# Performance work log

Hardware: AMD Instinct MI355X
Metric: run time of the kernel (lower is better)

## Reference

```python
import jax, jax.numpy as jnp
import numpy as np

DIM = 768
HEADS = 12
DIM_HEAD = DIM // HEADS  # 64
INNER = DIM_HEAD * HEADS  # 768
HIDDEN = 4 * DIM  # 3072
N = 31  # num_patches + 1, fixed by Block (num_patches=30)
B = 512
EPS = 1e-5
MASK_VAL = -987654321.0


def layernorm(x, g, b):
    mu = jnp.mean(x, axis=-1, keepdims=True)
    var = jnp.mean(jnp.square(x - mu), axis=-1, keepdims=True)
    return (x - mu) * jax.lax.rsqrt(var + EPS) * g + b


def setup_inputs() -> dict:
    key = jax.random.key(0)
    ks = jax.random.split(key, 12)
    s = 0.02
    return {
        "x": jax.random.normal(ks[0], (B, N, DIM), jnp.float32),
        "ln1_g": jnp.ones((DIM,), jnp.float32),
        "ln1_b": jnp.zeros((DIM,), jnp.float32),
        "w_qkv": jax.random.normal(ks[1], (DIM, 3 * INNER), jnp.float32) * s,
        "scale": jnp.full((HEADS,), DIM_HEAD ** -0.5, jnp.float32),
        "w_o": jax.random.normal(ks[2], (INNER, DIM), jnp.float32) * s,
        "b_o": jnp.zeros((DIM,), jnp.float32),
        "ln2_g": jnp.ones((DIM,), jnp.float32),
        "ln2_b": jnp.zeros((DIM,), jnp.float32),
        "w1": jax.random.normal(ks[3], (DIM, HIDDEN), jnp.float32) * s,
        "b1": jnp.zeros((HIDDEN,), jnp.float32),
        "w2": jax.random.normal(ks[4], (HIDDEN, DIM), jnp.float32) * s,
        "b2": jnp.zeros((DIM,), jnp.float32),
    }


def reference(x, ln1_g, ln1_b, w_qkv, scale, w_o, b_o, ln2_g, ln2_b, w1, b1, w2, b2):
    b, n, _ = x.shape
    # --- LSA attention ---
    h = layernorm(x, ln1_g, ln1_b)
    qkv = h @ w_qkv  # [b, n, 3*inner]
    q, k, v = jnp.split(qkv, 3, axis=-1)
    def split_heads(t):
        return t.reshape(b, n, HEADS, DIM_HEAD).transpose(0, 2, 1, 3)  # b h n d
    q, k, v = split_heads(q), split_heads(k), split_heads(v)
    dots = jnp.einsum('bhid,bhjd->bhij', q, k) * scale[None, :, None, None]
    # diagonal exclusion mask (self-token masked out)
    diag = jnp.eye(n, dtype=bool)
    dots = jnp.where(diag[None, None], MASK_VAL, dots)
    attn = jax.nn.softmax(dots, axis=-1)
    out = jnp.einsum('bhij,bhjd->bhid', attn, v)
    out = out.transpose(0, 2, 1, 3).reshape(b, n, INNER)
    x = x + out @ w_o + b_o
    # --- MLP ---
    h2 = layernorm(x, ln2_g, ln2_b)
    h2 = jax.nn.gelu(h2 @ w1 + b1, approximate=False)
    x = x + h2 @ w2 + b2
    return x
```

## Files before the change

kernel.cpp:

```cpp
#include <hip/hip_runtime.h>
#include <math.h>

#define DIM 768
#define HEADS 12
#define DHEAD 64
#define NTOK 31
#define BATCH 512
#define MTOK (BATCH * NTOK)
#define HIDDEN 3072
#define QKVN 2304
#define MASK_VAL -987654321.0f

typedef short s16x8 __attribute__((ext_vector_type(8)));
typedef float f32x4 __attribute__((ext_vector_type(4)));

static __device__ __forceinline__ float bs2f(unsigned short u) {
  unsigned int x = ((unsigned int)u) << 16;
  return __builtin_bit_cast(float, x);
}
static __device__ __forceinline__ unsigned short f2bs(float f) {
  unsigned int x = __builtin_bit_cast(unsigned int, f);
  x += 0x7fffu + ((x >> 16) & 1u);
  return (unsigned short)(x >> 16);
}

static __device__ __forceinline__ void gload16(const unsigned short* g, unsigned short* l) {
  __builtin_amdgcn_global_load_lds(
      (const __attribute__((address_space(1))) unsigned int*)g,
      (__attribute__((address_space(3))) unsigned int*)l, 16, 0, 0);
}

static __device__ __forceinline__ float epi_apply(int EPI, float v, int col, size_t idx,
                                                  const float* bias, const void* resid) {
  if (EPI == 0) return v;
  if (EPI == 2) {
    float t = v + bias[col];
    float arg = 1.5957691216f * t * (1.f + 0.044715f * t * t);
    return t * __builtin_amdgcn_rcpf(1.f + __expf(-arg));
  }
  if (EPI == 3) return v + bias[col] + ((const float*)resid)[idx];
  return v + bias[col] + bs2f(((const unsigned short*)resid)[idx]);
}

static __device__ __forceinline__ void epi_store(int EPI, void* outp, size_t idx, float t) {
  if (EPI == 4) ((float*)outp)[idx] = t;
  else ((unsigned short*)outp)[idx] = f2bs(t);
}

__global__ __launch_bounds__(256) void transpose_all_kernel(
    const float* __restrict__ w_qkv, const float* __restrict__ w_o,
    const float* __restrict__ w1, const float* __restrict__ w2,
    unsigned short* __restrict__ wqkvT, unsigned short* __restrict__ woT,
    unsigned short* __restrict__ w1T, unsigned short* __restrict__ w2T) {
  int t = blockIdx.x;
  const float* w;
  unsigned short* wt;
  int K, N, tx;
  if (t < 432) { w = w_qkv; wt = wqkvT; K = DIM; N = QKVN; tx = QKVN / 64; }
  else if (t < 576) { t -= 432; w = w_o; wt = woT; K = DIM; N = DIM; tx = DIM / 64; }
  else if (t < 1152) { t -= 576; w = w1; wt = w1T; K = DIM; N = HIDDEN; tx = HIDDEN / 64; }
  else { t -= 1152; w = w2; wt = w2T; K = HIDDEN; N = DIM; tx = DIM / 64; }
  int n0 = (t % tx) * 64, k0 = (t / tx) * 64;

  __shared__ float tl[64][65];
  int tid = threadIdx.x;
  int r = tid >> 4, c4 = (tid & 15) * 4;
#pragma unroll
  for (int i = 0; i < 4; ++i) {
    float4 v = *(const float4*)(w + (size_t)(k0 + r + i * 16) * N + n0 + c4);
    tl[r + i * 16][c4] = v.x;
    tl[r + i * 16][c4 + 1] = v.y;
    tl[r + i * 16][c4 + 2] = v.z;
    tl[r + i * 16][c4 + 3] = v.w;
  }
  __syncthreads();
#pragma unroll
  for (int i = 0; i < 4; ++i) {
    int n = r + i * 16;
    ushort4 o;
    o.x = f2bs(tl[c4 + 0][n]);
    o.y = f2bs(tl[c4 + 1][n]);
    o.z = f2bs(tl[c4 + 2][n]);
    o.w = f2bs(tl[c4 + 3][n]);
    *(ushort4*)(wt + (size_t)(n0 + n) * K + k0 + c4) = o;
  }
}

__global__ __launch_bounds__(256) void ln_kernel(const float* __restrict__ x,
                                                 const float* __restrict__ g,
                                                 const float* __restrict__ bta,
                                                 unsigned short* __restrict__ out) {
  int wid = threadIdx.x >> 6, lane = threadIdx.x & 63;
  size_t row = (size_t)blockIdx.x * 4 + wid;
  const float4* xr = (const float4*)(x + row * DIM);
  float4 v[3];
  v[0] = xr[lane];
  v[1] = xr[lane + 64];
  v[2] = xr[lane + 128];
  float s = 0.f, sq = 0.f;
#pragma unroll
  for (int i = 0; i < 3; ++i) {
    s += v[i].x + v[i].y + v[i].z + v[i].w;
    sq += v[i].x * v[i].x + v[i].y * v[i].y + v[i].z * v[i].z + v[i].w * v[i].w;
  }
#pragma unroll
  for (int off = 32; off; off >>= 1) {
    s += __shfl_xor(s, off);
    sq += __shfl_xor(sq, off);
  }
  float mu = s * (1.f / DIM);
  float var = sq * (1.f / DIM) - mu * mu;
  float rs = rsqrtf(var + 1e-5f);
#pragma unroll
  for (int i = 0; i < 3; ++i) {
    int col = i * 256 + lane * 4;
    float4 gg = *(const float4*)(g + col);
    float4 bb = *(const float4*)(bta + col);
    ushort4 o;
    o.x = f2bs((v[i].x - mu) * rs * gg.x + bb.x);
    o.y = f2bs((v[i].y - mu) * rs * gg.y + bb.y);
    o.z = f2bs((v[i].z - mu) * rs * gg.z + bb.z);
    o.w = f2bs((v[i].w - mu) * rs * gg.w + bb.w);
    *(ushort4*)(out + row * DIM + col) = o;
  }
}

__global__ __launch_bounds__(256) void ln_bf16_kernel(const unsigned short* __restrict__ x,
                                                      const float* __restrict__ g,
                                                      const float* __restrict__ bta,
                                                      unsigned short* __restrict__ out) {
  int wid = threadIdx.x >> 6, lane = threadIdx.x & 63;
  size_t row = (size_t)blockIdx.x * 4 + wid;
  const unsigned short* xr = x + row * DIM;
  float v[12];
#pragma unroll
  for (int i = 0; i < 3; ++i) {
    ushort4 u = *(const ushort4*)(xr + i * 256 + lane * 4);
    v[i * 4 + 0] = bs2f(u.x);
    v[i * 4 + 1] = bs2f(u.y);
    v[i * 4 + 2] = bs2f(u.z);
    v[i * 4 + 3] = bs2f(u.w);
  }
  float s = 0.f, sq = 0.f;
#pragma unroll
  for (int i = 0; i < 12; ++i) {
    s += v[i];
    sq += v[i] * v[i];
  }
#pragma unroll
  for (int off = 32; off; off >>= 1) {
    s += __shfl_xor(s, off);
    sq += __shfl_xor(sq, off);
  }
  float mu = s * (1.f / DIM);
  float var = sq * (1.f / DIM) - mu * mu;
  float rs = rsqrtf(var + 1e-5f);
#pragma unroll
  for (int i = 0; i < 3; ++i) {
    int col = i * 256 + lane * 4;
    float4 gg = *(const float4*)(g + col);
    float4 bb = *(const float4*)(bta + col);
    ushort4 o;
    o.x = f2bs((v[i * 4 + 0] - mu) * rs * gg.x + bb.x);
    o.y = f2bs((v[i * 4 + 1] - mu) * rs * gg.y + bb.y);
    o.z = f2bs((v[i * 4 + 2] - mu) * rs * gg.z + bb.z);
    o.w = f2bs((v[i * 4 + 3] - mu) * rs * gg.w + bb.w);
    *(ushort4*)(out + row * DIM + col) = o;
  }
}

template <int CMH, int CS, int CB, int RBUF, int RMH, int RKH, int RB, int VM, int NORD,
          typename STF>
__device__ __forceinline__ void gphP(const char* aB0, const char* bKH0, const char* bKH1,
                                     s16x8 (&af2)[2][4], s16x8 (&bk2)[2][3],
                                     f32x4 (&acc)[8][3], STF&& stage) {
  stage();
  if (VM == 2) asm volatile("s_waitcnt vmcnt(2)");
  if (VM == 0) asm volatile("s_waitcnt vmcnt(0)");
  __builtin_amdgcn_s_barrier();
  if (!NORD) {
    const char* aP = aB0 + RBUF * 32768 + RKH * 16384 + RMH * 4096;
#pragma unroll
    for (int mi = 0; mi < 4; ++mi) af2[CS ^ 1][mi] = *(const s16x8*)(aP + mi * 1024);
    if (RMH == 0) {
      const char* bp = (RKH ? bKH1 : bKH0) + RBUF * 24576;
#pragma unroll
      for (int ni = 0; ni < 3; ++ni) bk2[RB][ni] = *(const s16x8*)(bp + ni * 2048);
    }
  }
  __builtin_amdgcn_s_setprio(1);
#pragma unroll
  for (int mi = 0; mi < 4; ++mi)
#pragma unroll
    for (int ni = 0; ni < 3; ++ni)
      acc[CMH * 4 + mi][ni] = __builtin_amdgcn_mfma_f32_16x16x32_bf16(
          af2[CS][mi], bk2[CB][ni], acc[CMH * 4 + mi][ni], 0, 0, 0);
  __builtin_amdgcn_s_setprio(0);
  __builtin_amdgcn_s_barrier();
}

template <int EPI, int TPB>
__device__ __forceinline__ void gemm192_body(
    const unsigned short* __restrict__ A, const unsigned short* __restrict__ Bt,
    void* __restrict__ outp, const float* __restrict__ bias,
    const void* __restrict__ resid, int M, int N, int K, int ntn) {
  __shared__ char ldsc[114688];
  int tid = threadIdx.x;
  int lane = tid & 63, w = tid >> 6;
  int wm = w >> 2, wn = w & 3;
  int fr = lane & 15, q = lane >> 4;

  int nwg = gridDim.x, orig = blockIdx.x;
  int qd = nwg >> 3, r8 = nwg & 7, xcd = orig & 7, loc = orig >> 3;
  int bid = (xcd < r8 ? xcd * (qd + 1) : r8 * (qd + 1) + (xcd - r8) * qd) + loc;

  int rdoffA = (q * 16) ^ (((fr >> 1) & 3) << 4);
  const char* aB0 = ldsc + (wm * 128 + fr) * 64 + rdoffA;
  int brow0 = wn * 48 + fr;
  int bsw = brow0 & 7;
  const char* bBase = ldsc + 65536 + brow0 * 128 + (q ^ (bsw & 3)) * 16;
  const char* bKH0 = bBase + ((0 ^ (bsw >> 2)) * 64);
  const char* bKH1 = bBase + ((1 ^ (bsw >> 2)) * 64);

  int srow = tid >> 2;
  int seoffA = (((tid & 3) ^ ((srow >> 1) & 3))) << 3;
  size_t rstep = (size_t)K * 256;
  int NT = K / 64;

#pragma unroll 1
  for (int tl = 0; tl < TPB; ++tl) {
    int tile = bid * TPB + tl;
    int m0 = (tile / ntn) * 256, n0 = (tile % ntn) * 192;

    const char* Ab = (const char*)A + ((size_t)(m0 + srow) * K + seoffA) * 2;
    const char* Bb2 = (const char*)Bt +
        ((size_t)(n0 + (tid >> 3)) * K + (((tid & 7) ^ ((tid >> 3) & 7)) * 8)) * 2;

    auto stgA = [&](int kh, int buf, int t) {
      const char* gp = Ab + t * 128 + kh * 64;
      unsigned short* lp = (unsigned short*)(ldsc + buf * 32768 + kh * 16384 + w * 1024);
      gload16((const unsigned short*)gp, lp);
      gload16((const unsigned short*)(gp + rstep), (unsigned short*)((char*)lp + 8192));
    };
    auto stgB = [&](int j, int buf, int t) {
      gload16((const unsigned short*)(Bb2 + (size_t)j * 128 * K + t * 128),
              (unsigned short*)(ldsc + 65536 + buf * 24576 + j * 8192 + w * 1024));
    };
    auto nop = [&] {};

    f32x4 acc[8][3] = {};
    s16x8 af2[2][4], bk2[2][3];

    stgA(0, 0, 0);
    stgA(1, 0, 0);
    stgB(0, 0, 0);
    stgB(1, 0, 0);
    stgB(2, 0, 0);
    stgA(0, 1, 1);
    asm volatile("s_waitcnt vmcnt(2)");
    __builtin_amdgcn_s_barrier();
    {
#pragma unroll
      for (int mi = 0; mi < 4; ++mi) af2[0][mi] = *(const s16x8*)(aB0 + mi * 1024);
#pragma unroll
      for (int ni = 0; ni < 3; ++ni) bk2[0][ni] = *(const s16x8*)(bKH0 + ni * 2048);
    }

    for (int t = 0; t + 3 < NT; t += 2) {
      gphP<0, 0, 0, 0, 1, 0, 0, -1, 0>(aB0, bKH0, bKH1, af2, bk2, acc,
          [&] { stgA(1, 1, t + 1); stgB(0, 1, t + 1); stgB(1, 1, t + 1); });
      gphP<1, 1, 0, 0, 0, 1, 1, -1, 0>(aB0, bKH0, bKH1, af2, bk2, acc,
          [&] { stgB(2, 1, t + 1); });
      gphP<0, 0, 1, 0, 1, 1, 0, -1, 0>(aB0, bKH0, bKH1, af2, bk2, acc,
          [&] { stgA(0, 0, t + 2); });
      gphP<1, 1, 1, 1, 0, 0, 0, 2, 0>(aB0, bKH0, bKH1, af2, bk2, acc, nop);
      gphP<0, 0, 0, 1, 1, 0, 0, -1, 0>(aB0, bKH0, bKH1, af2, bk2, acc,
          [&] { stgA(1, 0, t + 2); stgB(0, 0, t + 2); stgB(1, 0, t + 2); });
      gphP<1, 1, 0, 1, 0, 1, 1, -1, 0>(aB0, bKH0, bKH1, af2, bk2, acc,
          [&] { stgB(2, 0, t + 2); });
      gphP<0, 0, 1, 1, 1, 1, 0, -1, 0>(aB0, bKH0, bKH1, af2, bk2, acc,
          [&] { stgA(0, 1, t + 3); });
      gphP<1, 1, 1, 0, 0, 0, 0, 2, 0>(aB0, bKH0, bKH1, af2, bk2, acc, nop);
    }
    gphP<0, 0, 0, 0, 1, 0, 0, -1, 0>(aB0, bKH0, bKH1, af2, bk2, acc,
        [&] { stgA(1, 1, NT - 1); stgB(0, 1, NT - 1); stgB(1, 1, NT - 1); });
    gphP<1, 1, 0, 0, 0, 1, 1, -1, 0>(aB0, bKH0, bKH1, af2, bk2, acc,
        [&] { stgB(2, 1, NT - 1); });
    gphP<0, 0, 1, 0, 1, 1, 0, -1, 0>(aB0, bKH0, bKH1, af2, bk2, acc, nop);
    gphP<1, 1, 1, 1, 0, 0, 0, 0, 0>(aB0, bKH0, bKH1, af2, bk2, acc, nop);
    gphP<0, 0, 0, 1, 1, 0, 0, -1, 0>(aB0, bKH0, bKH1, af2, bk2, acc, nop);
    gphP<1, 1, 0, 1, 0, 1, 1, -1, 0>(aB0, bKH0, bKH1, af2, bk2, acc, nop);
    gphP<0, 0, 1, 1, 1, 1, 0, -1, 0>(aB0, bKH0, bKH1, af2, bk2, acc, nop);
    gphP<1, 1, 1, 0, 0, 0, 0, -1, 1>(aB0, bKH0, bKH1, af2, bk2, acc, nop);

#pragma unroll
    for (int am = 0; am < 8; ++am)
#pragma unroll
      for (int ni = 0; ni < 3; ++ni)
#pragma unroll
        for (int rr = 0; rr < 4; ++rr) {
          int row = m0 + wm * 128 + am * 16 + q * 4 + rr;
          int col = n0 + wn * 48 + ni * 16 + fr;
          size_t idx = (size_t)row * N + col;
          epi_store(EPI, outp, idx, epi_apply(EPI, acc[am][ni][rr], col, idx, bias, resid));
        }
  }
}

__global__ __launch_bounds__(512, 2) void gemm_qkv(const unsigned short* A,
                                                   const unsigned short* Bt, void* o,
                                                   const float* b, const void* r, int M,
                                                   int N, int K, int ntn) {
  gemm192_body<0, 3>(A, Bt, o, b, r, M, N, K, ntn);
}
__global__ __launch_bounds__(512, 2) void gemm_mlp1(const unsigned short* A,
                                                    const unsigned short* Bt, void* o,
                                                    const float* b, const void* r, int M,
                                                    int N, int K, int ntn) {
  gemm192_body<2, 4>(A, Bt, o, b, r, M, N, K, ntn);
}
__global__ __launch_bounds__(512, 2) void gemm_proj(const unsigned short* A,
                                                    const unsigned short* Bt, void* o,
                                                    const float* b, const void* r, int M,
                                                    int N, int K, int ntn) {
  gemm192_body<3, 1>(A, Bt, o, b, r, M, N, K, ntn);
}
__global__ __launch_bounds__(512, 2) void gemm_mlp2(const unsigned short* A,
                                                    const unsigned short* Bt, void* o,
                                                    const float* b, const void* r, int M,
                                                    int N, int K, int ntn) {
  gemm192_body<4, 1>(A, Bt, o, b, r, M, N, K, ntn);
}

__global__ __launch_bounds__(256) void attn_mfma_kernel(const unsigned short* __restrict__ qkv,
                                                        const float* __restrict__ scale,
                                                        unsigned short* __restrict__ ao) {
  __shared__ unsigned short Vt[4][64][40];
  __shared__ unsigned short Pl[4][32][32];
  int wid = threadIdx.x >> 6, lane = threadIdx.x & 63;
  int pair = blockIdx.x * 4 + wid;
  int b = pair / HEADS, h = pair % HEADS;
  const unsigned short* base = qkv + (size_t)b * NTOK * QKVN + h * DHEAD;
  const unsigned short* Qp = base;
  const unsigned short* Kp = base + 768;
  const unsigned short* Vp = base + 1536;

  int c = lane & 15, q = lane >> 4;
  int oct = q * 8;

  unsigned short vcol[NTOK];
#pragma unroll
  for (int j = 0; j < NTOK; ++j) vcol[j] = Vp[(size_t)j * QKVN + lane];
#pragma unroll
  for (int j = 0; j < NTOK; ++j) Vt[wid][lane][j] = vcol[j];
  Vt[wid][lane][31] = 0;

  s16x8 kf[2][2] = {{{0}}}, qf[2][2] = {{{0}}};
#pragma unroll
  for (int t = 0; t < 2; ++t) {
    int row = t * 16 + c;
    if (row < NTOK) {
#pragma unroll
      for (int s = 0; s < 2; ++s) {
        kf[t][s] = *(const s16x8*)(Kp + (size_t)row * QKVN + s * 32 + oct);
        qf[t][s] = *(const s16x8*)(Qp + (size_t)row * QKVN + s * 32 + oct);
      }
    }
  }

  f32x4 st[2][2] = {};
#pragma unroll
  for (int jt = 0; jt < 2; ++jt)
#pragma unroll
    for (int it = 0; it < 2; ++it)
#pragma unroll
      for (int s = 0; s < 2; ++s)
        st[jt][it] =
            __builtin_amdgcn_mfma_f32_16x16x32_bf16(kf[jt][s], qf[it][s], st[jt][it], 0, 0, 0);

  float scl = scale[h];
  float p[2][2][4];
#pragma unroll
  for (int it = 0; it < 2; ++it)
#pragma unroll
    for (int jt = 0; jt < 2; ++jt)
#pragma unroll
      for (int r = 0; r < 4; ++r) {
        int j = jt * 16 + 4 * q + r;
        int i = it * 16 + c;
        float v = st[jt][it][r] * scl;
        if (j == 31 || j == i) v = MASK_VAL;
        p[it][jt][r] = v;
      }
#pragma unroll
  for (int it = 0; it < 2; ++it) {
    float m = p[it][0][0];
#pragma unroll
    for (int jt = 0; jt < 2; ++jt)
#pragma unroll
      for (int r = 0; r < 4; ++r) m = fmaxf(m, p[it][jt][r]);
    m = fmaxf(m, __shfl_xor(m, 16));
    m = fmaxf(m, __shfl_xor(m, 32));
    float s = 0.f;
#pragma unroll
    for (int jt = 0; jt < 2; ++jt)
#pragma unroll
      for (int r = 0; r < 4; ++r) {
        float e = __expf(p[it][jt][r] - m);
        p[it][jt][r] = e;
        s += e;
      }
    s += __shfl_xor(s, 16);
    s += __shfl_xor(s, 32);
    float inv = __builtin_amdgcn_rcpf(s);
#pragma unroll
    for (int jt = 0; jt < 2; ++jt)
#pragma unroll
      for (int r = 0; r < 4; ++r) p[it][jt][r] *= inv;
  }
#pragma unroll
  for (int it = 0; it < 2; ++it)
#pragma unroll
    for (int jt = 0; jt < 2; ++jt) {
      unsigned int w0 =
          (unsigned int)f2bs(p[it][jt][0]) | ((unsigned int)f2bs(p[it][jt][1]) << 16);
      unsigned int w1 =
          (unsigned int)f2bs(p[it][jt][2]) | ((unsigned int)f2bs(p[it][jt][3]) << 16);
      uint2 pk = {w0, w1};
      *(uint2*)&Pl[wid][it * 16 + c][jt * 16 + 4 * q] = pk;
    }

  s16x8 pa[2];
#pragma unroll
  for (int it = 0; it < 2; ++it) pa[it] = *(const s16x8*)&Pl[wid][it * 16 + c][oct];
  f32x4 o[2][4];
#pragma unroll
  for (int it = 0; it < 2; ++it)
#pragma unroll
    for (int dt = 0; dt < 4; ++dt) {
      s16x8 vb = *(const s16x8*)&Vt[wid][dt * 16 + c][oct];
      f32x4 z = {0.f, 0.f, 0.f, 0.f};
      o[it][dt] = __builtin_amdgcn_mfma_f32_16x16x32_bf16(pa[it], vb, z, 0, 0, 0);
    }
#pragma unroll
  for (int it = 0; it < 2; ++it)
#pragma unroll
    for (int r = 0; r < 4; ++r) {
      int i = it * 16 + 4 * q + r;
      if (i < NTOK) {
        size_t rowoff = ((size_t)b * NTOK + i) * DIM + h * DHEAD;
#pragma unroll
        for (int dt = 0; dt < 4; ++dt) ao[rowoff + dt * 16 + c] = f2bs(o[it][dt][r]);
      }
    }
}

extern "C" void kernel_launch(void* const* d_in, const int* in_sizes, int n_in,
                              void* d_out, int out_size, void* d_ws, size_t ws_size,
                              hipStream_t stream) {
  (void)in_sizes; (void)n_in; (void)out_size; (void)ws_size;
  const float* x = (const float*)d_in[0];
  const float* ln1_g = (const float*)d_in[1];
  const float* ln1_b = (const float*)d_in[2];
  const float* w_qkv = (const float*)d_in[3];
  const float* scale = (const float*)d_in[4];
  const float* w_o = (const float*)d_in[5];
  const float* b_o = (const float*)d_in[6];
  const float* ln2_g = (const float*)d_in[7];
  const float* ln2_b = (const float*)d_in[8];
  const float* w1 = (const float*)d_in[9];
  const float* b1 = (const float*)d_in[10];
  const float* w2 = (const float*)d_in[11];
  const float* b2 = (const float*)d_in[12];

  char* ws = (char*)d_ws;
  unsigned short* buf1 = (unsigned short*)(ws + 0);
  unsigned short* qkv_bf = (unsigned short*)(ws + 24379392);
  unsigned short* x2 = (unsigned short*)(ws + 24379392);
  unsigned short* g_bf = (unsigned short*)(ws + 97517568);
  unsigned short* wqkvT = (unsigned short*)(ws + 195035136);
  unsigned short* woT = (unsigned short*)(ws + 198574080);
  unsigned short* w1T = (unsigned short*)(ws + 199753728);
  unsigned short* w2T = (unsigned short*)(ws + 204472320);

  transpose_all_kernel<<<1728, 256, 0, stream>>>(w_qkv, w_o, w1, w2, wqkvT, woT, w1T, w2T);

  ln_kernel<<<MTOK / 4, 256, 0, stream>>>(x, ln1_g, ln1_b, buf1);
  gemm_qkv<<<248, 512, 0, stream>>>(
      buf1, wqkvT, qkv_bf, nullptr, nullptr, MTOK, QKVN, DIM, QKVN / 192);
  attn_mfma_kernel<<<(BATCH * HEADS) / 4, 256, 0, stream>>>(qkv_bf, scale, buf1);
  gemm_proj<<<248, 512, 0, stream>>>(
      buf1, woT, x2, b_o, x, MTOK, DIM, DIM, DIM / 192);
  ln_bf16_kernel<<<MTOK / 4, 256, 0, stream>>>(x2, ln2_g, ln2_b, buf1);
  gemm_mlp1<<<248, 512, 0, stream>>>(
      buf1, w1T, g_bf, b1, nullptr, MTOK, HIDDEN, DIM, HIDDEN / 192);
  gemm_mlp2<<<248, 512, 0, stream>>>(
      g_bf, w2T, (float*)d_out, b2, x2, MTOK, DIM, HIDDEN, DIM / 192);
}
```

Baseline: 310.4 us.

## Add 256x256-tile GEMM body and use it for the MLP up-projection

Adds a new GEMM body that computes 256x256 output tiles with a double-buffered, 128KB LDS staging pipeline. Global loads for upcoming k-steps are interleaved with MFMA phases, using explicit vmcnt waits and barriers. The MLP first-layer GEMM switches to it, with 3 tiles per block instead of 4 tiles of 256x192. The aim is more operand reuse per loaded byte and fewer tile iterations. The cost is a larger accumulator and LDS footprint, which raises register-spill and occupancy risk under the 512-thread, 2-block launch bound.

```diff
diff --git a/kernel.cpp b/kernel.cpp
--- a/kernel.cpp
+++ b/kernel.cpp
@@ -307,6 +307,139 @@
   }
 }
 
+template <int CMH, int CS, int CB, int RBUF, int RMH, int RKH, int RB, int VM, int NORD,
+          typename STF>
+__device__ __forceinline__ void gphQ(const char* aB0, const char* bB0,
+                                     s16x8 (&af2)[2][4], s16x8 (&bk2)[2][4],
+                                     f32x4 (&acc)[8][4], STF&& stage) {
+  stage();
+  if (VM == 10) asm volatile("s_waitcnt vmcnt(10)");
+  if (VM == 4) asm volatile("s_waitcnt vmcnt(4)");
+  if (VM == 0) asm volatile("s_waitcnt vmcnt(0)");
+  __builtin_amdgcn_s_barrier();
+  if (!NORD) {
+    const char* aP = aB0 + RBUF * 32768 + RKH * 16384 + RMH * 4096;
+#pragma unroll
+    for (int mi = 0; mi < 4; ++mi) af2[CS ^ 1][mi] = *(const s16x8*)(aP + mi * 1024);
+    if (RMH == 0) {
+      const char* bP = bB0 + RBUF * 32768 + RKH * 16384;
+#pragma unroll
+      for (int ni = 0; ni < 4; ++ni) bk2[RB][ni] = *(const s16x8*)(bP + ni * 1024);
+    }
+  }
+  __builtin_amdgcn_s_setprio(1);
+#pragma unroll
+  for (int mi = 0; mi < 4; ++mi)
+#pragma unroll
+    for (int ni = 0; ni < 4; ++ni)
+      acc[CMH * 4 + mi][ni] = __builtin_amdgcn_mfma_f32_16x16x32_bf16(
+          af2[CS][mi], bk2[CB][ni], acc[CMH * 4 + mi][ni], 0, 0, 0);
+  __builtin_amdgcn_s_setprio(0);
+  __builtin_amdgcn_s_barrier();
+}
+
+template <int EPI, int TPB>
+__device__ __forceinline__ void gemm256_body(
+    const unsigned short* __restrict__ A, const unsigned short* __restrict__ Bt,
+    void* __restrict__ outp, const float* __restrict__ bias,
+    const void* __restrict__ resid, int M, int N, int K, int ntn) {
+  __shared__ char ldsc[131072];
+  int tid = threadIdx.x;
+  int lane = tid & 63, w = tid >> 6;
+  int wm = w >> 2, wn = w & 3;
+  int fr = lane & 15, q = lane >> 4;
+
+  int nwg = gridDim.x, orig = blockIdx.x;
+  int qd = nwg >> 3, r8 = nwg & 7, xcd = orig & 7, loc = orig >> 3;
+  int bid = (xcd < r8 ? xcd * (qd + 1) : r8 * (qd + 1) + (xcd - r8) * qd) + loc;
+
+  int rdoff = (q * 16) ^ (((fr >> 1) & 3) << 4);
+  const char* aB0 = ldsc + (wm * 128 + fr) * 64 + rdoff;
+  const char* bB0 = ldsc + 65536 + (wn * 64 + fr) * 64 + rdoff;
+
+  int srow = tid >> 2;
+  int seoff = (((tid & 3) ^ ((srow >> 1) & 3))) << 3;
+  size_t rstep = (size_t)K * 256;
+  int NT = K / 64;
+
+#pragma unroll 1
+  for (int tl = 0; tl < TPB; ++tl) {
+    int tile = bid * TPB + tl;
+    int m0 = (tile / ntn) * 256, n0 = (tile % ntn) * 256;
+
+    const char* Ab = (const char*)A + ((size_t)(m0 + srow) * K + seoff) * 2;
+    const char* Bb = (const char*)Bt + ((size_t)(n0 + srow) * K + seoff) * 2;
+
+    auto stg = [&](int mat, int kh, int buf, int t) {
+      const char* gp = (mat ? Bb : Ab) + t * 128 + kh * 64;
+      unsigned short* lp =
+          (unsigned short*)(ldsc + mat * 65536 + buf * 32768 + kh * 16384 + w * 1024);
+      gload16((const unsigned short*)gp, lp);
+      gload16((const unsigned short*)(gp + rstep), (unsigned short*)((char*)lp + 8192));
+    };
+    auto nop = [&] {};
+
+    f32x4 acc[8][4] = {};
+    s16x8 af2[2][4], bk2[2][4];
+
+    stg(1, 0, 0, 0);
+    stg(0, 0, 0, 0);
+    stg(1, 1, 0, 0);
+    stg(0, 1, 0, 0);
+    stg(1, 0, 1, 1);
+    stg(0, 0, 1, 1);
+    stg(1, 1, 1, 1);
+    asm volatile("s_waitcnt vmcnt(6)");
+    __builtin_amdgcn_s_barrier();
+    {
+#pragma unroll
+      for (int mi = 0; mi < 4; ++mi) af2[0][mi] = *(const s16x8*)(aB0 + mi * 1024);
+#pragma unroll
+      for (int ni = 0; ni < 4; ++ni) bk2[0][ni] = *(const s16x8*)(bB0 + ni * 1024);
+    }
+
+    for (int t = 0; t + 3 < NT; t += 2) {
+      gphQ<0, 0, 0, 0, 1, 0, 0, -1, 0>(aB0, bB0, af2, bk2, acc,
+          [&] { stg(0, 1, 1, t + 1); });
+      gphQ<1, 1, 0, 0, 0, 1, 1, 10, 0>(aB0, bB0, af2, bk2, acc,
+          [&] { stg(1, 0, 0, t + 2); });
+      gphQ<0, 0, 1, 0, 1, 1, 0, -1, 0>(aB0, bB0, af2, bk2, acc,
+          [&] { stg(0, 0, 0, t + 2); });
+      gphQ<1, 1, 1, 1, 0, 0, 0, 10, 0>(aB0, bB0, af2, bk2, acc,
+          [&] { stg(1, 1, 0, t + 2); });
+      gphQ<0, 0, 0, 1, 1, 0, 0, -1, 0>(aB0, bB0, af2, bk2, acc,
+          [&] { stg(0, 1, 0, t + 2); });
+      gphQ<1, 1, 0, 1, 0, 1, 1, 10, 0>(aB0, bB0, af2, bk2, acc,
+          [&] { stg(1, 0, 1, t + 3); });
+      gphQ<0, 0, 1, 1, 1, 1, 0, -1, 0>(aB0, bB0, af2, bk2, acc,
+          [&] { stg(0, 0, 1, t + 3); });
+      gphQ<1, 1, 1, 0, 0, 0, 0, 10, 0>(aB0, bB0, af2, bk2, acc,
+          [&] { stg(1, 1, 1, t + 3); });
+    }
+    gphQ<0, 0, 0, 0, 1, 0, 0, -1, 0>(aB0, bB0, af2, bk2, acc,
+        [&] { stg(0, 1, 1, NT - 1); });
+    gphQ<1, 1, 0, 0, 0, 1, 1, -1, 0>(aB0, bB0, af2, bk2, acc, nop);
+    gphQ<0, 0, 1, 0, 1, 1, 0, -1, 0>(aB0, bB0, af2, bk2, acc, nop);
+    gphQ<1, 1, 1, 1, 0, 0, 0, 4, 0>(aB0, bB0, af2, bk2, acc, nop);
+    gphQ<0, 0, 0, 1, 1, 0, 0, -1, 0>(aB0, bB0, af2, bk2, acc, nop);
+    gphQ<1, 1, 0, 1, 0, 1, 1, 0, 0>(aB0, bB0, af2, bk2, acc, nop);
+    gphQ<0, 0, 1, 1, 1, 1, 0, -1, 0>(aB0, bB0, af2, bk2, acc, nop);
+    gphQ<1, 1, 1, 0, 0, 0, 0, -1, 1>(aB0, bB0, af2, bk2, acc, nop);
+
+#pragma unroll
+    for (int am = 0; am < 8; ++am)
+#pragma unroll
+      for (int ni = 0; ni < 4; ++ni)
+#pragma unroll
+        for (int rr = 0; rr < 4; ++rr) {
+          int row = m0 + wm * 128 + am * 16 + q * 4 + rr;
+          int col = n0 + wn * 64 + ni * 16 + fr;
+          size_t idx = (size_t)row * N + col;
+          epi_store(EPI, outp, idx, epi_apply(EPI, acc[am][ni][rr], col, idx, bias, resid));
+        }
+  }
+}
+
 __global__ __launch_bounds__(512, 2) void gemm_qkv(const unsigned short* A,
                                                    const unsigned short* Bt, void* o,
                                                    const float* b, const void* r, int M,
@@ -317,7 +450,7 @@
                                                     const unsigned short* Bt, void* o,
                                                     const float* b, const void* r, int M,
                                                     int N, int K, int ntn) {
-  gemm192_body<2, 4>(A, Bt, o, b, r, M, N, K, ntn);
+  gemm256_body<2, 3>(A, Bt, o, b, r, M, N, K, ntn);
 }
 __global__ __launch_bounds__(512, 2) void gemm_proj(const unsigned short* A,
                                                     const unsigned short* Bt, void* o,
@@ -493,7 +626,7 @@
       buf1, woT, x2, b_o, x, MTOK, DIM, DIM, DIM / 192);
   ln_bf16_kernel<<<MTOK / 4, 256, 0, stream>>>(x2, ln2_g, ln2_b, buf1);
   gemm_mlp1<<<248, 512, 0, stream>>>(
-      buf1, w1T, g_bf, b1, nullptr, MTOK, HIDDEN, DIM, HIDDEN / 192);
+      buf1, w1T, g_bf, b1, nullptr, MTOK, HIDDEN, DIM, HIDDEN / 256);
   gemm_mlp2<<<248, 512, 0, stream>>>(
       g_bf, w2T, (float*)d_out, b2, x2, MTOK, DIM, HIDDEN, DIM / 192);
 }
```

New measurement: 308.3 us (median of 2 runs). Within noise of the previous version (-0.7%).

## Use 256x256 tile GEMM with 32x32x16 MFMA for first MLP layer

Applied to the files above, without the earlier changes.

Adds a new GEMM body that computes 256x256 output tiles per workgroup, using 32x32x16 bf16 MFMA instructions and a double-buffered 128KB LDS pipeline staged through global_load_lds. The MLP1 GEMM switches to it, covering 3 tiles per block across 248 blocks. Larger tiles raise arithmetic intensity and the bigger MFMA shape cuts LDS reads per flop. In exchange, 128KB of LDS per block limits occupancy, and tile coverage depends on M being divisible by 256.

```diff
diff --git a/kernel.cpp b/kernel.cpp
--- a/kernel.cpp
+++ b/kernel.cpp
@@ -13,6 +13,7 @@
 
 typedef short s16x8 __attribute__((ext_vector_type(8)));
 typedef float f32x4 __attribute__((ext_vector_type(4)));
+typedef float f32x16 __attribute__((ext_vector_type(16)));
 
 static __device__ __forceinline__ float bs2f(unsigned short u) {
   unsigned int x = ((unsigned int)u) << 16;
@@ -307,6 +308,126 @@
   }
 }
 
+template <int BUF, int KH, int VM, typename STF>
+__device__ __forceinline__ void gph32(const char* aB, const char* bB, int o0, int o1,
+                                      f32x16 (&acc)[4][2], STF&& stage) {
+  const char* aP = aB + BUF * 32768 + KH * 16384;
+  const char* bP = bB + BUF * 32768 + KH * 16384;
+  s16x8 af[4][2], bk[2][2];
+#pragma unroll
+  for (int mt = 0; mt < 4; ++mt) {
+    af[mt][0] = *(const s16x8*)(aP + mt * 2048 + o0);
+    af[mt][1] = *(const s16x8*)(aP + mt * 2048 + o1);
+  }
+#pragma unroll
+  for (int nt = 0; nt < 2; ++nt) {
+    bk[nt][0] = *(const s16x8*)(bP + nt * 2048 + o0);
+    bk[nt][1] = *(const s16x8*)(bP + nt * 2048 + o1);
+  }
+  stage();
+  if (VM == 8) asm volatile("s_waitcnt vmcnt(8)");
+  if (VM == 4) asm volatile("s_waitcnt vmcnt(4)");
+  if (VM == 0) asm volatile("s_waitcnt vmcnt(0)");
+  __builtin_amdgcn_s_barrier();
+  asm volatile("s_waitcnt lgkmcnt(0)");
+  __builtin_amdgcn_s_setprio(1);
+#pragma unroll
+  for (int mt = 0; mt < 4; ++mt)
+#pragma unroll
+    for (int nt = 0; nt < 2; ++nt) {
+      acc[mt][nt] =
+          __builtin_amdgcn_mfma_f32_32x32x16_bf16(af[mt][0], bk[nt][0], acc[mt][nt], 0, 0, 0);
+      acc[mt][nt] =
+          __builtin_amdgcn_mfma_f32_32x32x16_bf16(af[mt][1], bk[nt][1], acc[mt][nt], 0, 0, 0);
+    }
+  __builtin_amdgcn_s_setprio(0);
+  __builtin_amdgcn_s_barrier();
+}
+
+template <int EPI, int TPB>
+__device__ __forceinline__ void gemm256x_body(
+    const unsigned short* __restrict__ A, const unsigned short* __restrict__ Bt,
+    void* __restrict__ outp, const float* __restrict__ bias,
+    const void* __restrict__ resid, int M, int N, int K, int ntn) {
+  __shared__ char ldsc[131072];
+  int tid = threadIdx.x;
+  int lane = tid & 63, w = tid >> 6;
+  int wm = w >> 2, wn = w & 3;
+  int l31 = lane & 31, lh = lane >> 5;
+
+  int nwg = gridDim.x, orig = blockIdx.x;
+  int qd = nwg >> 3, r8 = nwg & 7, xcd = orig & 7, loc = orig >> 3;
+  int bid = (xcd < r8 ? xcd * (qd + 1) : r8 * (qd + 1) + (xcd - r8) * qd) + loc;
+
+  int swz = ((l31 >> 1) & 3) ^ ((l31 >> 3) & 3);
+  int o0 = ((0 + lh) ^ swz) * 16;
+  int o1 = ((2 + lh) ^ swz) * 16;
+  const char* aB = ldsc + (wm * 128 + l31) * 64;
+  const char* bB = ldsc + 65536 + (wn * 64 + l31) * 64;
+
+  int srow = tid >> 2;
+  int seoff = (((tid & 3) ^ ((srow >> 1) & 3) ^ ((srow >> 3) & 3))) << 3;
+  size_t rstep = (size_t)K * 256;
+  int NT = K / 64;
+
+#pragma unroll 1
+  for (int tl = 0; tl < TPB; ++tl) {
+    int tile = bid * TPB + tl;
+    int m0 = (tile / ntn) * 256, n0 = (tile % ntn) * 256;
+
+    const char* Ab = (const char*)A + ((size_t)(m0 + srow) * K + seoff) * 2;
+    const char* Bb = (const char*)Bt + ((size_t)(n0 + srow) * K + seoff) * 2;
+
+    auto stg = [&](int mat, int kh, int buf, int t) {
+      const char* gp = (mat ? Bb : Ab) + t * 128 + kh * 64;
+      unsigned short* lp =
+          (unsigned short*)(ldsc + mat * 65536 + buf * 32768 + kh * 16384 + w * 1024);
+      gload16((const unsigned short*)gp, lp);
+      gload16((const unsigned short*)(gp + rstep), (unsigned short*)((char*)lp + 8192));
+    };
+    auto nop = [&] {};
+
+    f32x16 acc[4][2] = {};
+
+    stg(1, 0, 0, 0);
+    stg(0, 0, 0, 0);
+    stg(1, 1, 0, 0);
+    stg(0, 1, 0, 0);
+    stg(1, 0, 1, 1);
+    stg(0, 0, 1, 1);
+    asm volatile("s_waitcnt vmcnt(8)");
+    __builtin_amdgcn_s_barrier();
+
+    for (int t = 0; t + 3 < NT; t += 2) {
+      gph32<0, 0, 8>(aB, bB, o0, o1, acc,
+                     [&] { stg(0, 1, 1, t + 1); stg(1, 1, 1, t + 1); });
+      gph32<0, 1, 8>(aB, bB, o0, o1, acc,
+                     [&] { stg(1, 0, 0, t + 2); stg(0, 0, 0, t + 2); });
+      gph32<1, 0, 8>(aB, bB, o0, o1, acc,
+                     [&] { stg(1, 1, 0, t + 2); stg(0, 1, 0, t + 2); });
+      gph32<1, 1, 8>(aB, bB, o0, o1, acc,
+                     [&] { stg(1, 0, 1, t + 3); stg(0, 0, 1, t + 3); });
+    }
+    gph32<0, 0, 8>(aB, bB, o0, o1, acc,
+                   [&] { stg(0, 1, 1, NT - 1); stg(1, 1, 1, NT - 1); });
+    gph32<0, 1, 4>(aB, bB, o0, o1, acc, nop);
+    gph32<1, 0, 0>(aB, bB, o0, o1, acc, nop);
+    gph32<1, 1, -1>(aB, bB, o0, o1, acc, nop);
+
+#pragma unroll
+    for (int mt = 0; mt < 4; ++mt)
+#pragma unroll
+      for (int nt = 0; nt < 2; ++nt)
+#pragma unroll
+        for (int reg = 0; reg < 16; ++reg) {
+          int row = m0 + wm * 128 + mt * 32 + (reg & 3) + 8 * (reg >> 2) + 4 * lh;
+          int col = n0 + wn * 64 + nt * 32 + l31;
+          size_t idx = (size_t)row * N + col;
+          epi_store(EPI, outp, idx, epi_apply(EPI, acc[mt][nt][reg], col, idx, bias, resid));
+        }
+  }
+}
+
 __global__ __launch_bounds__(512, 2) void gemm_qkv(const unsigned short* A,
                                                    const unsigned short* Bt, void* o,
                                                    const float* b, const void* r, int M,
@@ -317,7 +438,7 @@
                                                     const unsigned short* Bt, void* o,
                                                     const float* b, const void* r, int M,
                                                     int N, int K, int ntn) {
-  gemm192_body<2, 4>(A, Bt, o, b, r, M, N, K, ntn);
+  gemm256x_body<2, 3>(A, Bt, o, b, r, M, N, K, ntn);
 }
 __global__ __launch_bounds__(512, 2) void gemm_proj(const unsigned short* A,
                                                     const unsigned short* Bt, void* o,
@@ -493,7 +614,7 @@
       buf1, woT, x2, b_o, x, MTOK, DIM, DIM, DIM / 192);
   ln_bf16_kernel<<<MTOK / 4, 256, 0, stream>>>(x2, ln2_g, ln2_b, buf1);
   gemm_mlp1<<<248, 512, 0, stream>>>(
-      buf1, w1T, g_bf, b1, nullptr, MTOK, HIDDEN, DIM, HIDDEN / 192);
+      buf1, w1T, g_bf, b1, nullptr, MTOK, HIDDEN, DIM, HIDDEN / 256);
   gemm_mlp2<<<248, 512, 0, stream>>>(
       g_bf, w2T, (float*)d_out, b2, x2, MTOK, DIM, HIDDEN, DIM / 192);
 }
```

New measurement: 316.2 us. No clear change (+1.9%).
